# Kernel optimization log

Measured on AMD Instinct MI355X. Metric: run time of the kernel, lower is better.

## Reference

```python
import jax, jax.numpy as jnp
import numpy as np

K = 4096
D = 64
DECAY = 0.99
EPS = 1e-05


def setup_inputs() -> dict:
    key = jax.random.key(0)
    k1, k2 = jax.random.split(key)
    z_e = jax.random.normal(k1, (32, 1024, D), dtype=jnp.float32)
    emb = jax.random.normal(k2, (K, D), dtype=jnp.float32)
    emb = emb / jnp.clip(jnp.linalg.norm(emb, axis=1, keepdims=True), 1e-8)
    return {
        "z_e": z_e,
        "embedding": emb,
        "ema_cluster_size": jnp.zeros((K,), jnp.float32),
        "ema_embedding": jnp.zeros((K, D), jnp.float32),
    }


def reference(z_e, embedding, ema_cluster_size, ema_embedding):
    B, L, Dd = z_e.shape
    flat = z_e.reshape(-1, Dd)                                   # (N, D)
    flat_norm = flat / jnp.clip(jnp.linalg.norm(flat, axis=1, keepdims=True), 1e-8)
    dots = flat_norm @ embedding.T                               # (N, K)
    indices = jnp.argmax(dots, axis=1)                           # (N,)
    z_q = embedding[indices].reshape(B, L, Dd)
    z_q_st = z_e + jax.lax.stop_gradient(z_q - z_e)

    # ---- usage / stats ----
    usage = jnp.zeros((K,), jnp.float32).at[indices].add(1.0)    # bincount
    probs = usage / jnp.maximum(usage.sum(), 1.0)
    safe = jnp.where(probs > 0, probs, 1.0)
    perplexity = jnp.exp(-jnp.sum(probs * jnp.log(safe)))
    dead_ratio = jnp.mean((usage == 0).astype(jnp.float32))
    stats = jnp.stack([perplexity, dead_ratio])

    # ---- EMA update (training-mode buffer math, functional) ----
    fn = jax.lax.stop_gradient(flat_norm)
    embed_sum = jnp.zeros((K, Dd), jnp.float32).at[indices].add(fn)  # one_hot.T @ flat_norm
    new_cs = DECAY * ema_cluster_size + (1.0 - DECAY) * usage
    new_ema_emb = DECAY * ema_embedding + (1.0 - DECAY) * embed_sum
    n = new_cs.sum()
    smoothed = (new_cs + EPS) / (n + K * EPS)
    norm_e = new_ema_emb / jnp.clip(smoothed, EPS)[:, None]
    norm_e = norm_e / jnp.clip(jnp.linalg.norm(norm_e, axis=1, keepdims=True), 1e-8)

    # ---- dead-code reinit (reinit_prob=1.0, threshold=0); deterministic key ----
    N = fn.shape[0]
    rand_idx = jax.random.randint(jax.random.key(1), (K,), 0, N)
    src = fn[rand_idx]
    src = src / jnp.clip(jnp.linalg.norm(src, axis=1, keepdims=True), 1e-8)
    dead = usage <= 0.0
    new_embedding = jnp.where(dead[:, None], src, norm_e)

    return (z_q_st, z_q, indices.reshape(B, L), stats,
            new_embedding, new_cs, new_ema_emb)
```

## Files before the change

### kernel.cpp

```cpp
#include <hip/hip_runtime.h>
#include <math.h>

#define N_TOK 32768
#define KCB   4096
#define SPLITS 6

#define OFF_ZQST   0
#define OFF_ZQ     2097152
#define OFF_IDX    4194304
#define OFF_STATS  4227072
#define OFF_NEWEMB 4227074
#define OFF_NEWCS  4489218
#define OFF_NEWEMA 4493314

#define WS_FN       0
#define WS_ESUM     8388608
#define WS_USAGE    9437184
#define WS_CNTS     9453568
#define WS_FULLKEY  9454592
#define WS_EHI      9716736
#define WS_ELO      10241024
#define WS_PK1      10765312
#define WS_PK2      11551744
#define WS_IDXW     12338176
#define WS_RIDX     12469248
#define WS_FULL     12485632

#define THRKEY 131072u
#define DGRKEY 98304u

typedef __attribute__((ext_vector_type(8))) short short8;
typedef __attribute__((ext_vector_type(4))) float float4v;

__device__ __forceinline__ float wave_sum(float v) {
#pragma unroll
  for (int off = 32; off > 0; off >>= 1) v += __shfl_xor(v, off, 64);
  return v;
}

__device__ __forceinline__ unsigned short f2bf(float f) {
  unsigned u = __float_as_uint(f);
  unsigned r = (u + 0x7fffu + ((u >> 16) & 1u)) >> 16;
  return (unsigned short)r;
}
__device__ __forceinline__ float bf2f(unsigned short h) {
  return __uint_as_float(((unsigned)h) << 16);
}

typedef const __attribute__((address_space(1))) unsigned int* gas_ptr;
typedef __attribute__((address_space(3))) unsigned int* las_ptr;
__device__ __forceinline__ void gl_lds16(const void* g, void* l) {
  __builtin_amdgcn_global_load_lds((gas_ptr)g, (las_ptr)l, 16, 0, 0);
}

__device__ __forceinline__ unsigned rotl32(unsigned x, int d) {
  return (x << d) | (x >> (32 - d));
}
__device__ __forceinline__ void tf2x32(unsigned k0, unsigned k1,
                                       unsigned x0, unsigned x1,
                                       unsigned& o0, unsigned& o1) {
  unsigned ks2 = k0 ^ k1 ^ 0x1BD11BDAu;
  unsigned v0 = x0 + k0, v1 = x1 + k1;
  v0 += v1; v1 = rotl32(v1, 13) ^ v0;
  v0 += v1; v1 = rotl32(v1, 15) ^ v0;
  v0 += v1; v1 = rotl32(v1, 26) ^ v0;
  v0 += v1; v1 = rotl32(v1, 6) ^ v0;
  v0 += k1; v1 += ks2 + 1u;
  v0 += v1; v1 = rotl32(v1, 17) ^ v0;
  v0 += v1; v1 = rotl32(v1, 29) ^ v0;
  v0 += v1; v1 = rotl32(v1, 16) ^ v0;
  v0 += v1; v1 = rotl32(v1, 24) ^ v0;
  v0 += ks2; v1 += k0 + 2u;
  v0 += v1; v1 = rotl32(v1, 13) ^ v0;
  v0 += v1; v1 = rotl32(v1, 15) ^ v0;
  v0 += v1; v1 = rotl32(v1, 26) ^ v0;
  v0 += v1; v1 = rotl32(v1, 6) ^ v0;
  v0 += k0; v1 += k1 + 3u;
  v0 += v1; v1 = rotl32(v1, 17) ^ v0;
  v0 += v1; v1 = rotl32(v1, 29) ^ v0;
  v0 += v1; v1 = rotl32(v1, 16) ^ v0;
  v0 += v1; v1 = rotl32(v1, 24) ^ v0;
  v0 += k1; v1 += ks2 + 4u;
  v0 += v1; v1 = rotl32(v1, 13) ^ v0;
  v0 += v1; v1 = rotl32(v1, 15) ^ v0;
  v0 += v1; v1 = rotl32(v1, 26) ^ v0;
  v0 += v1; v1 = rotl32(v1, 6) ^ v0;
  v0 += ks2; v1 += k0 + 5u;
  o0 = v0; o1 = v1;
}

__global__ __launch_bounds__(256) void k_prep(const float* __restrict__ z_e,
                                              const float* __restrict__ emb,
                                              float* __restrict__ fn,
                                              unsigned short* __restrict__ ehi,
                                              unsigned short* __restrict__ elo,
                                              int* __restrict__ ridx,
                                              int* __restrict__ zbase) {
  int b = blockIdx.x;
  int t = threadIdx.x;
  if (b < 8192) {
    int n = b * 4 + (t >> 6);
    int lane = t & 63;
    float x = z_e[n * 64 + lane];
    float ss = wave_sum(x * x);
    fn[n * 64 + lane] = x / fmaxf(sqrtf(ss), 1e-8f);
  } else if (b < 9216) {
    int i = (b - 8192) * 256 + t;
    float x = emb[i];
    unsigned short h = f2bf(x);
    ehi[i] = h;
    elo[i] = f2bf(x - bf2f(h));
  } else if (b < 9224) {
    int j = (b - 9216) * 256 + t;
    unsigned a0, b0, a1, b1;
    tf2x32(0u, 1u, 0u, 2u, a0, b0);
    tf2x32(0u, 1u, 1u, 3u, a1, b1);
    unsigned o0, o1;
    tf2x32(b0, b1, (unsigned)j, (unsigned)(j + 2048), o0, o1);
    ridx[j] = (int)(o0 & 32767u);
    ridx[j + 2048] = (int)(o1 & 32767u);
  } else {
    int i = (b - 9224) * 256 + t;
    zbase[i] = 0;
  }
}

__global__ __launch_bounds__(256, 3) void k_dots(const float* __restrict__ fn,
                                                 const unsigned short* __restrict__ ehi,
                                                 const unsigned short* __restrict__ elo,
                                                 unsigned* __restrict__ pk1,
                                                 unsigned* __restrict__ pk2) {
  __shared__ unsigned short lds_b[2][2][2][1024];
  int t = threadIdx.x;
  int wave = t >> 6, lane = t & 63;
  int g = lane >> 4, n = lane & 15;
  int qw = blockIdx.x * 256 + wave * 64;
  int split = blockIdx.y;
  int nt16 = (split < 2) ? 704 : 672;
  int tstart16 = (split < 3) ? 704 * split : 672 * split + 64;
  int ntiles = nt16 >> 4;
  int npairs = ntiles >> 1;

  short8 ahi[4][2], alo[4][2];
#pragma unroll
  for (int s = 0; s < 4; s++)
#pragma unroll
    for (int ks = 0; ks < 2; ks++) {
      const float* src = fn + (qw + s * 16 + n) * 64 + ks * 32 + g * 8;
      short8 h, l;
#pragma unroll
      for (int j = 0; j < 8; j++) {
        float f = src[j] * 0.25f;
        unsigned short hu = f2bf(f);
        h[j] = (short)hu;
        l[j] = (short)f2bf(f - bf2f(hu));
      }
      ahi[s][ks] = h;
      alo[s][ks] = l;
    }

  unsigned run1[4][4], run2[4][4];
#pragma unroll
  for (int s = 0; s < 4; s++)
#pragma unroll
    for (int r = 0; r < 4; r++) { run1[s][r] = 0u; run2[s][r] = 0u; }

  const float hiclamp = __uint_as_float(0x3F9FFFFFu);

  int stile = wave >> 1;
  int shl = wave & 1;
  const unsigned short* sbase = shl ? elo : ehi;
  int c0 = lane ^ ((lane >> 3) & 7);

#define STAGE(BUF, PAIR)                                                        \
    {                                                                           \
      const unsigned short* sg =                                                \
          sbase + (tstart16 + ((PAIR) * 2 + stile) * 16) * 64;                  \
      gl_lds16(sg + c0 * 8, &lds_b[BUF][stile][shl][0]);                        \
      gl_lds16(sg + 512 + c0 * 8, &lds_b[BUF][stile][shl][512]);                \
    }

  int sh0 = (n * 8 + (g ^ (n & 7))) * 8;
  int sh1 = (n * 8 + ((g + 4) ^ (n & 7))) * 8;

#define MFMA_BLOCK(H0, H1, L0, L1)                                              \
    float4v a0 = (float4v){1.125f, 1.125f, 1.125f, 1.125f};                     \
    float4v a1 = a0, a2 = a0, a3 = a0;                                          \
    a0 = __builtin_amdgcn_mfma_f32_16x16x32_bf16(alo[0][0], H0, a0, 0, 0, 0);   \
    a1 = __builtin_amdgcn_mfma_f32_16x16x32_bf16(alo[1][0], H0, a1, 0, 0, 0);   \
    a2 = __builtin_amdgcn_mfma_f32_16x16x32_bf16(alo[2][0], H0, a2, 0, 0, 0);   \
    a3 = __builtin_amdgcn_mfma_f32_16x16x32_bf16(alo[3][0], H0, a3, 0, 0, 0);   \
    a0 = __builtin_amdgcn_mfma_f32_16x16x32_bf16(alo[0][1], H1, a0, 0, 0, 0);   \
    a1 = __builtin_amdgcn_mfma_f32_16x16x32_bf16(alo[1][1], H1, a1, 0, 0, 0);   \
    a2 = __builtin_amdgcn_mfma_f32_16x16x32_bf16(alo[2][1], H1, a2, 0, 0, 0);   \
    a3 = __builtin_amdgcn_mfma_f32_16x16x32_bf16(alo[3][1], H1, a3, 0, 0, 0);   \
    a0 = __builtin_amdgcn_mfma_f32_16x16x32_bf16(ahi[0][0], L0, a0, 0, 0, 0);   \
    a1 = __builtin_amdgcn_mfma_f32_16x16x32_bf16(ahi[1][0], L0, a1, 0, 0, 0);   \
    a2 = __builtin_amdgcn_mfma_f32_16x16x32_bf16(ahi[2][0], L0, a2, 0, 0, 0);   \
    a3 = __builtin_amdgcn_mfma_f32_16x16x32_bf16(ahi[3][0], L0, a3, 0, 0, 0);   \
    a0 = __builtin_amdgcn_mfma_f32_16x16x32_bf16(ahi[0][1], L1, a0, 0, 0, 0);   \
    a1 = __builtin_amdgcn_mfma_f32_16x16x32_bf16(ahi[1][1], L1, a1, 0, 0, 0);   \
    a2 = __builtin_amdgcn_mfma_f32_16x16x32_bf16(ahi[2][1], L1, a2, 0, 0, 0);   \
    a3 = __builtin_amdgcn_mfma_f32_16x16x32_bf16(ahi[3][1], L1, a3, 0, 0, 0);   \
    a0 = __builtin_amdgcn_mfma_f32_16x16x32_bf16(ahi[0][0], H0, a0, 0, 0, 0);   \
    a1 = __builtin_amdgcn_mfma_f32_16x16x32_bf16(ahi[1][0], H0, a1, 0, 0, 0);   \
    a2 = __builtin_amdgcn_mfma_f32_16x16x32_bf16(ahi[2][0], H0, a2, 0, 0, 0);   \
    a3 = __builtin_amdgcn_mfma_f32_16x16x32_bf16(ahi[3][0], H0, a3, 0, 0, 0);   \
    a0 = __builtin_amdgcn_mfma_f32_16x16x32_bf16(ahi[0][1], H1, a0, 0, 0, 0);   \
    a1 = __builtin_amdgcn_mfma_f32_16x16x32_bf16(ahi[1][1], H1, a1, 0, 0, 0);   \
    a2 = __builtin_amdgcn_mfma_f32_16x16x32_bf16(ahi[2][1], H1, a2, 0, 0, 0);   \
    a3 = __builtin_amdgcn_mfma_f32_16x16x32_bf16(ahi[3][1], H1, a3, 0, 0, 0);

#define SELECT_BLOCK(KT)                                                        \
    {                                                                           \
      unsigned invb = (unsigned)(nt16 - 1 - (KT) * 16 - n);                     \
      _Pragma("unroll") for (int r = 0; r < 4; r++) {                           \
        float x0 = __builtin_amdgcn_fmed3f(a0[r], 1.0f, hiclamp);               \
        unsigned kb0 = (__float_as_uint(x0) << 10) + invb;                      \
        run2[0][r] = max(run2[0][r], min(run1[0][r], kb0));                     \
        run1[0][r] = max(run1[0][r], kb0);                                      \
        float x1 = __builtin_amdgcn_fmed3f(a1[r], 1.0f, hiclamp);               \
        unsigned kb1 = (__float_as_uint(x1) << 10) + invb;                      \
        run2[1][r] = max(run2[1][r], min(run1[1][r], kb1));                     \
        run1[1][r] = max(run1[1][r], kb1);                                      \
        float x2 = __builtin_amdgcn_fmed3f(a2[r], 1.0f, hiclamp);               \
        unsigned kb2 = (__float_as_uint(x2) << 10) + invb;                      \
        run2[2][r] = max(run2[2][r], min(run1[2][r], kb2));                     \
        run1[2][r] = max(run1[2][r], kb2);                                      \
        float x3 = __builtin_amdgcn_fmed3f(a3[r], 1.0f, hiclamp);               \
        unsigned kb3 = (__float_as_uint(x3) << 10) + invb;                      \
        run2[3][r] = max(run2[3][r], min(run1[3][r], kb3));                     \
        run1[3][r] = max(run1[3][r], kb3);                                      \
      }                                                                         \
    }

  STAGE(0, 0)
  __syncthreads();
  int bb = 0;
#pragma unroll 1
  for (int p = 0; p < npairs; p++) {
    if (p + 1 < npairs) STAGE(bb ^ 1, p + 1)
    {
      short8 H0 = *(const short8*)&lds_b[bb][0][0][sh0];
      short8 H1 = *(const short8*)&lds_b[bb][0][0][sh1];
      short8 L0 = *(const short8*)&lds_b[bb][0][1][sh0];
      short8 L1 = *(const short8*)&lds_b[bb][0][1][sh1];
      MFMA_BLOCK(H0, H1, L0, L1)
      SELECT_BLOCK(p * 2)
    }
    {
      short8 H0 = *(const short8*)&lds_b[bb][1][0][sh0];
      short8 H1 = *(const short8*)&lds_b[bb][1][0][sh1];
      short8 L0 = *(const short8*)&lds_b[bb][1][1][sh0];
      short8 L1 = *(const short8*)&lds_b[bb][1][1][sh1];
      MFMA_BLOCK(H0, H1, L0, L1)
      SELECT_BLOCK(p * 2 + 1)
    }
    __syncthreads();
    bb ^= 1;
  }
#undef MFMA_BLOCK
#undef SELECT_BLOCK
#undef STAGE

#pragma unroll
  for (int off = 1; off <= 8; off <<= 1) {
#pragma unroll
    for (int s = 0; s < 4; s++)
#pragma unroll
      for (int r = 0; r < 4; r++) {
        unsigned o1 = (unsigned)__shfl_xor((int)run1[s][r], off, 64);
        unsigned o2 = (unsigned)__shfl_xor((int)run2[s][r], off, 64);
        run2[s][r] = max(min(run1[s][r], o1), max(run2[s][r], o2));
        run1[s][r] = max(run1[s][r], o1);
      }
  }

  if (n == 0) {
#pragma unroll
    for (int s = 0; s < 4; s++)
#pragma unroll
      for (int r = 0; r < 4; r++) {
        int q = qw + s * 16 + g * 4 + r;
        pk1[split * N_TOK + q] = run1[s][r];
        pk2[split * N_TOK + q] = run2[s][r];
      }
  }
}

__global__ __launch_bounds__(256) void k_merge_fix(const unsigned* __restrict__ pk1,
                                                   const unsigned* __restrict__ pk2,
                                                   const float* __restrict__ fn,
                                                   const float* __restrict__ emb,
                                                   int* __restrict__ idxw,
                                                   int* __restrict__ cnts,
                                                   int* __restrict__ full,
                                                   unsigned long long* __restrict__ fullkey) {
  __shared__ int nfl;
  __shared__ int fl[256][13];
  int t = threadIdx.x;
  if (t == 0) nfl = 0;
  __syncthreads();
  int q = blockIdx.x * 256 + t;
  unsigned k1v[SPLITS], k2v[SPLITS];
  unsigned b1 = 0u, b2 = 0u;
  int s1 = 0;
#pragma unroll
  for (int s = 0; s < SPLITS; s++) {
    unsigned k1 = pk1[s * N_TOK + q];
    unsigned k2 = pk2[s * N_TOK + q];
    k1v[s] = k1;
    k2v[s] = k2;
    b2 = max(b2, min(b1, k1));
    b2 = max(b2, k2);
    if (k1 > b1) { b1 = k1; s1 = s; }
  }
  int nt16s = (s1 < 2) ? 704 : 672;
  int ts16 = (s1 < 3) ? 704 * s1 : 672 * s1 + 64;
  idxw[q] = ts16 + nt16s - 1 - (int)(b1 & 1023u);
  fullkey[q] = 0ull;
  bool danger = false;
#pragma unroll
  for (int s = 0; s < SPLITS; s++) danger |= (k2v[s] + DGRKEY > b1);
  if (danger) {
    int p = atomicAdd(&cnts[0], 1);
    full[p] = q;
  } else if (b1 - b2 < THRKEY) {
    int p = atomicAdd(&nfl, 1);
    fl[p][0] = q;
#pragma unroll
    for (int s = 0; s < SPLITS; s++) {
      int nt = (s < 2) ? 704 : 672;
      int tss = (s < 3) ? 704 * s : 672 * s + 64;
      fl[p][1 + s] = tss + nt - 1 - (int)(k1v[s] & 1023u);
      fl[p][7 + s] = tss + nt - 1 - (int)(k2v[s] & 1023u);
    }
  }
  __syncthreads();
  int m = nfl;
  int wave = t >> 6, lane = t & 63;
  int c = lane >> 2, dg = lane & 3;
  for (int i = wave; i < m; i += 4) {
    int fq = fl[i][0];
    int code = (c < 12) ? fl[i][1 + c] : fl[i][1];
    const float* er = emb + code * 64 + dg * 16;
    const float* fr = fn + fq * 64 + dg * 16;
    double d = 0.0;
#pragma unroll
    for (int k = 0; k < 16; k++) d += (double)er[k] * (double)fr[k];
    d += __shfl_xor(d, 1, 64);
    d += __shfl_xor(d, 2, 64);
    unsigned long long key =
        ((unsigned long long)__double_as_longlong(d + 2.0) & ~0xFFFULL) |
        (unsigned long long)(4095 - code);
    if (c >= 12) key = 0ull;
#pragma unroll
    for (int off = 4; off <= 32; off <<= 1) {
      unsigned long long o = __shfl_xor(key, off, 64);
      key = key > o ? key : o;
    }
    if (lane == 0) idxw[fq] = 4095 - (int)(key & 0xFFFULL);
  }
}

__global__ __launch_bounds__(256) void k_fix_full(const int* __restrict__ cnts,
                                                  const int* __restrict__ full,
                                                  const float* __restrict__ fn,
                                                  const float* __restrict__ emb,
                                                  unsigned long long* __restrict__ fullkey) {
  __shared__ float sfn[64];
  __shared__ unsigned long long red[256];
  int t = threadIdx.x;
  int chunk = blockIdx.x & 15;
  int c = chunk * 256 + t;
  float cr[64];
  {
    const float4v* er4 = (const float4v*)(emb + c * 64);
#pragma unroll
    for (int kk = 0; kk < 16; kk++) {
      float4v v = er4[kk];
      cr[kk * 4 + 0] = v[0];
      cr[kk * 4 + 1] = v[1];
      cr[kk * 4 + 2] = v[2];
      cr[kk * 4 + 3] = v[3];
    }
  }
  int total = cnts[0];
  total = total < N_TOK ? total : N_TOK;
  int qstride = (int)(gridDim.x >> 4);
  for (int w = (int)(blockIdx.x >> 4); w < total; w += qstride) {
    int q = full[w];
    __syncthreads();
    if (t < 64) sfn[t] = fn[q * 64 + t];
    __syncthreads();
    double s0 = 0, s1 = 0, s2 = 0, s3 = 0;
#pragma unroll
    for (int k = 0; k < 16; k++) {
      s0 += (double)cr[k] * (double)sfn[k];
      s1 += (double)cr[k + 16] * (double)sfn[k + 16];
      s2 += (double)cr[k + 32] * (double)sfn[k + 32];
      s3 += (double)cr[k + 48] * (double)sfn[k + 48];
    }
    double d = (s0 + s1) + (s2 + s3);
    unsigned long long key =
        ((unsigned long long)__double_as_longlong(d + 2.0) & ~0xFFFULL) |
        (unsigned long long)(4095 - c);
    red[t] = key;
    __syncthreads();
    for (int s = 128; s > 0; s >>= 1) {
      if (t < s) red[t] = red[t] > red[t + s] ? red[t] : red[t + s];
      __syncthreads();
    }
    if (t == 0) atomicMax(&fullkey[q], red[0]);
  }
}

__global__ __launch_bounds__(256) void k_write_scatter(const int* __restrict__ idxw,
                                                       const unsigned long long* __restrict__ fullkey,
                                                       const float* __restrict__ z_e,
                                                       const float* __restrict__ emb,
                                                       const float* __restrict__ fn,
                                                       float* __restrict__ out,
                                                       float* __restrict__ esum,
                                                       float* __restrict__ usage) {
  int t = threadIdx.x;
  int nn = blockIdx.x * 4 + (t >> 6);
  int lane = t & 63;
  unsigned long long fk = fullkey[nn];
  int bi = fk ? (4095 - (int)(fk & 0xFFFULL)) : idxw[nn];
  float v = emb[bi * 64 + lane];
  float ze = z_e[nn * 64 + lane];
  out[OFF_ZQST + nn * 64 + lane] = ze + (v - ze);
  out[OFF_ZQ + nn * 64 + lane] = v;
  atomicAdd(&esum[bi * 64 + lane], fn[nn * 64 + lane]);
  if (lane == 0) {
    out[OFF_IDX + nn] = (float)bi;
    atomicAdd(&usage[bi], 1.0f);
  }
}

__global__ __launch_bounds__(256) void k_stats(const float* __restrict__ usage,
                                               const float* __restrict__ ema_cs,
                                               float* __restrict__ scal) {
  __shared__ float rE[4], rD[4], rC[4];
  int t = threadIdx.x;
  int i = blockIdx.x * 256 + t;
  float u = usage[i];
  float p = u * (1.0f / 32768.0f);
  float ent = (p > 0.f) ? p * logf(p) : 0.f;
  float dead = (u == 0.f) ? 1.f : 0.f;
  float cs = 0.99f * ema_cs[i] + 0.01f * u;
  ent = wave_sum(ent);
  dead = wave_sum(dead);
  cs = wave_sum(cs);
  int w = t >> 6, lane = t & 63;
  if (lane == 0) { rE[w] = ent; rD[w] = dead; rC[w] = cs; }
  __syncthreads();
  if (t == 0) {
    atomicAdd(&scal[0], rE[0] + rE[1] + rE[2] + rE[3]);
    atomicAdd(&scal[1], rD[0] + rD[1] + rD[2] + rD[3]);
    atomicAdd(&scal[2], rC[0] + rC[1] + rC[2] + rC[3]);
  }
}

__global__ __launch_bounds__(256) void k_final(const float* __restrict__ usage,
                                               const float* __restrict__ ema_cs,
                                               const float* __restrict__ ema_emb,
                                               const float* __restrict__ esum,
                                               const float* __restrict__ fn,
                                               const int* __restrict__ ridx,
                                               const float* __restrict__ scal,
                                               float* __restrict__ out) {
  int t = threadIdx.x;
  int k = blockIdx.x * 4 + (t >> 6);
  int lane = t & 63;
  if (blockIdx.x == 0 && t == 0) {
    out[OFF_STATS + 0] = expf(-scal[0]);
    out[OFF_STATS + 1] = scal[1] * (1.0f / 4096.0f);
  }
  float u = usage[k];
  float ncs = 0.99f * ema_cs[k] + 0.01f * u;
  if (lane == 0) out[OFF_NEWCS + k] = ncs;
  float nee = 0.99f * ema_emb[k * 64 + lane] + 0.01f * esum[k * 64 + lane];
  out[OFF_NEWEMA + k * 64 + lane] = nee;

  float n = scal[2];
  float smoothed = (ncs + 1e-5f) / (n + 4096.0f * 1e-5f);
  float ne = nee / fmaxf(smoothed, 1e-5f);
  float ss = wave_sum(ne * ne);
  ne = ne / fmaxf(sqrtf(ss), 1e-8f);

  float res;
  if (u <= 0.f) {
    int rsrc = ridx[k];
    float v = fn[rsrc * 64 + lane];
    float s2 = wave_sum(v * v);
    res = v / fmaxf(sqrtf(s2), 1e-8f);
  } else {
    res = ne;
  }
  out[OFF_NEWEMB + k * 64 + lane] = res;
}

extern "C" void kernel_launch(void* const* d_in, const int* in_sizes, int n_in,
                              void* d_out, int out_size, void* d_ws, size_t ws_size,
                              hipStream_t stream) {
  const float* z_e = (const float*)d_in[0];
  const float* emb = (const float*)d_in[1];
  const float* ema_cs = (const float*)d_in[2];
  const float* ema_emb = (const float*)d_in[3];
  float* out = (float*)d_out;
  char* ws = (char*)d_ws;

  float* fn = (float*)(ws + WS_FN);
  float* esum = (float*)(ws + WS_ESUM);
  float* usage = (float*)(ws + WS_USAGE);
  int* cnts = (int*)(ws + WS_CNTS);
  float* scal = (float*)(ws + WS_CNTS + 16);
  unsigned long long* fullkey = (unsigned long long*)(ws + WS_FULLKEY);
  unsigned short* ehi = (unsigned short*)(ws + WS_EHI);
  unsigned short* elo = (unsigned short*)(ws + WS_ELO);
  unsigned* pk1 = (unsigned*)(ws + WS_PK1);
  unsigned* pk2 = (unsigned*)(ws + WS_PK2);
  int* idxw = (int*)(ws + WS_IDXW);
  int* ridx = (int*)(ws + WS_RIDX);
  int* full = (int*)(ws + WS_FULL);

  k_prep<<<10265, 256, 0, stream>>>(z_e, emb, fn, ehi, elo, ridx, (int*)(ws + WS_ESUM));
  k_dots<<<dim3(128, SPLITS), 256, 0, stream>>>(fn, ehi, elo, pk1, pk2);
  k_merge_fix<<<128, 256, 0, stream>>>(pk1, pk2, fn, emb, idxw, cnts, full, fullkey);
  k_fix_full<<<1024, 256, 0, stream>>>(cnts, full, fn, emb, fullkey);
  k_write_scatter<<<8192, 256, 0, stream>>>(idxw, fullkey, z_e, emb, fn, out, esum, usage);
  k_stats<<<16, 256, 0, stream>>>(usage, ema_cs, scal);
  k_final<<<1024, 256, 0, stream>>>(usage, ema_cs, ema_emb, esum, fn, ridx, scal, out);
}
```

Before: 156.4 us.

## Fold stats kernel into prep and final kernels; use med3 for top-2 tracking

Removes the separate k_stats launch. The cluster-size total is computed in k_prep from ema_cs alone, relying on usage summing to exactly N (0.01*32768 = 327.68). Entropy and dead ratio are now computed by an extra block in k_final. In the k_dots selection loop, the max/min pair that tracks the second-best key is replaced with a single v_med3_u32 through inline asm. The cost removed is one kernel launch plus the global atomics that fed the scalar stats.

```diff
diff --git a/kernel.cpp b/kernel.cpp
--- a/kernel.cpp
+++ b/kernel.cpp
@@ -51,6 +51,12 @@
 typedef __attribute__((address_space(3))) unsigned int* las_ptr;
 __device__ __forceinline__ void gl_lds16(const void* g, void* l) {
   __builtin_amdgcn_global_load_lds((gas_ptr)g, (las_ptr)l, 16, 0, 0);
+}
+
+__device__ __forceinline__ unsigned med3u(unsigned a, unsigned b, unsigned c) {
+  unsigned r;
+  asm("v_med3_u32 %0, %1, %2, %3" : "=v"(r) : "v"(a), "v"(b), "v"(c));
+  return r;
 }
 
 __device__ __forceinline__ unsigned rotl32(unsigned x, int d) {
@@ -91,11 +97,14 @@
 
 __global__ __launch_bounds__(256) void k_prep(const float* __restrict__ z_e,
                                               const float* __restrict__ emb,
+                                              const float* __restrict__ ema_cs,
                                               float* __restrict__ fn,
                                               unsigned short* __restrict__ ehi,
                                               unsigned short* __restrict__ elo,
                                               int* __restrict__ ridx,
-                                              int* __restrict__ zbase) {
+                                              int* __restrict__ zbase,
+                                              float* __restrict__ scal) {
+  __shared__ float rC[4];
   int b = blockIdx.x;
   int t = threadIdx.x;
   if (b < 8192) {
@@ -122,6 +131,17 @@
   } else {
     int i = (b - 9224) * 256 + t;
     zbase[i] = 0;
+    if (b == 10264) {
+      __syncthreads();
+      float s = 0.f;
+#pragma unroll
+      for (int j = 0; j < 16; j++) s += ema_cs[j * 256 + t];
+      s = wave_sum(s);
+      int w = t >> 6, lane = t & 63;
+      if (lane == 0) rC[w] = s;
+      __syncthreads();
+      if (t == 0) scal[2] = 0.99f * (rC[0] + rC[1] + rC[2] + rC[3]) + 327.68f;
+    }
   }
 }
 
@@ -217,19 +237,19 @@
       _Pragma("unroll") for (int r = 0; r < 4; r++) {                           \
         float x0 = __builtin_amdgcn_fmed3f(a0[r], 1.0f, hiclamp);               \
         unsigned kb0 = (__float_as_uint(x0) << 10) + invb;                      \
-        run2[0][r] = max(run2[0][r], min(run1[0][r], kb0));                     \
+        run2[0][r] = med3u(run1[0][r], run2[0][r], kb0);                        \
         run1[0][r] = max(run1[0][r], kb0);                                      \
         float x1 = __builtin_amdgcn_fmed3f(a1[r], 1.0f, hiclamp);               \
         unsigned kb1 = (__float_as_uint(x1) << 10) + invb;                      \
-        run2[1][r] = max(run2[1][r], min(run1[1][r], kb1));                     \
+        run2[1][r] = med3u(run1[1][r], run2[1][r], kb1);                        \
         run1[1][r] = max(run1[1][r], kb1);                                      \
         float x2 = __builtin_amdgcn_fmed3f(a2[r], 1.0f, hiclamp);               \
         unsigned kb2 = (__float_as_uint(x2) << 10) + invb;                      \
-        run2[2][r] = max(run2[2][r], min(run1[2][r], kb2));                     \
+        run2[2][r] = med3u(run1[2][r], run2[2][r], kb2);                        \
         run1[2][r] = max(run1[2][r], kb2);                                      \
         float x3 = __builtin_amdgcn_fmed3f(a3[r], 1.0f, hiclamp);               \
         unsigned kb3 = (__float_as_uint(x3) << 10) + invb;                      \
-        run2[3][r] = max(run2[3][r], min(run1[3][r], kb3));                     \
+        run2[3][r] = med3u(run1[3][r], run2[3][r], kb3);                        \
         run1[3][r] = max(run1[3][r], kb3);                                      \
       }                                                                         \
     }
@@ -439,30 +459,6 @@
   }
 }
 
-__global__ __launch_bounds__(256) void k_stats(const float* __restrict__ usage,
-                                               const float* __restrict__ ema_cs,
-                                               float* __restrict__ scal) {
-  __shared__ float rE[4], rD[4], rC[4];
-  int t = threadIdx.x;
-  int i = blockIdx.x * 256 + t;
-  float u = usage[i];
-  float p = u * (1.0f / 32768.0f);
-  float ent = (p > 0.f) ? p * logf(p) : 0.f;
-  float dead = (u == 0.f) ? 1.f : 0.f;
-  float cs = 0.99f * ema_cs[i] + 0.01f * u;
-  ent = wave_sum(ent);
-  dead = wave_sum(dead);
-  cs = wave_sum(cs);
-  int w = t >> 6, lane = t & 63;
-  if (lane == 0) { rE[w] = ent; rD[w] = dead; rC[w] = cs; }
-  __syncthreads();
-  if (t == 0) {
-    atomicAdd(&scal[0], rE[0] + rE[1] + rE[2] + rE[3]);
-    atomicAdd(&scal[1], rD[0] + rD[1] + rD[2] + rD[3]);
-    atomicAdd(&scal[2], rC[0] + rC[1] + rC[2] + rC[3]);
-  }
-}
-
 __global__ __launch_bounds__(256) void k_final(const float* __restrict__ usage,
                                                const float* __restrict__ ema_cs,
                                                const float* __restrict__ ema_emb,
@@ -472,12 +468,29 @@
                                                const float* __restrict__ scal,
                                                float* __restrict__ out) {
   int t = threadIdx.x;
+  if (blockIdx.x == 1024) {
+    __shared__ float rE[4], rD[4];
+    float ent = 0.f, dead = 0.f;
+#pragma unroll
+    for (int j = 0; j < 16; j++) {
+      float u = usage[j * 256 + t];
+      float p = u * (1.0f / 32768.0f);
+      ent += (p > 0.f) ? p * logf(p) : 0.f;
+      dead += (u == 0.f) ? 1.f : 0.f;
+    }
+    ent = wave_sum(ent);
+    dead = wave_sum(dead);
+    int w = t >> 6, lane = t & 63;
+    if (lane == 0) { rE[w] = ent; rD[w] = dead; }
+    __syncthreads();
+    if (t == 0) {
+      out[OFF_STATS + 0] = expf(-(rE[0] + rE[1] + rE[2] + rE[3]));
+      out[OFF_STATS + 1] = (rD[0] + rD[1] + rD[2] + rD[3]) * (1.0f / 4096.0f);
+    }
+    return;
+  }
   int k = blockIdx.x * 4 + (t >> 6);
   int lane = t & 63;
-  if (blockIdx.x == 0 && t == 0) {
-    out[OFF_STATS + 0] = expf(-scal[0]);
-    out[OFF_STATS + 1] = scal[1] * (1.0f / 4096.0f);
-  }
   float u = usage[k];
   float ncs = 0.99f * ema_cs[k] + 0.01f * u;
   if (lane == 0) out[OFF_NEWCS + k] = ncs;
@@ -526,11 +539,11 @@
   int* ridx = (int*)(ws + WS_RIDX);
   int* full = (int*)(ws + WS_FULL);
 
-  k_prep<<<10265, 256, 0, stream>>>(z_e, emb, fn, ehi, elo, ridx, (int*)(ws + WS_ESUM));
+  k_prep<<<10265, 256, 0, stream>>>(z_e, emb, ema_cs, fn, ehi, elo, ridx,
+                                    (int*)(ws + WS_ESUM), scal);
   k_dots<<<dim3(128, SPLITS), 256, 0, stream>>>(fn, ehi, elo, pk1, pk2);
   k_merge_fix<<<128, 256, 0, stream>>>(pk1, pk2, fn, emb, idxw, cnts, full, fullkey);
   k_fix_full<<<1024, 256, 0, stream>>>(cnts, full, fn, emb, fullkey);
   k_write_scatter<<<8192, 256, 0, stream>>>(idxw, fullkey, z_e, emb, fn, out, esum, usage);
-  k_stats<<<16, 256, 0, stream>>>(usage, ema_cs, scal);
-  k_final<<<1024, 256, 0, stream>>>(usage, ema_cs, ema_emb, esum, fn, ridx, scal, out);
-}
+  k_final<<<1025, 256, 0, stream>>>(usage, ema_cs, ema_emb, esum, fn, ridx, scal, out);
+}
```

Result: faster. 151.6 us (-3.1%).
